# Kernel tuning notes

Measured on AMD Instinct MI355X. Metric: run time of the kernel, lower is better.

## Reference

```python
import jax, jax.numpy as jnp
import numpy as np

B, S, D, E, K = 2, 2048, 1024, 8, 2
H = 4 * D  # FFN hidden


def setup_inputs() -> dict:
    key = jax.random.key(0)
    ks = jax.random.split(key, 6)
    x = jax.random.normal(ks[0], (B, S, D), dtype=jnp.float32)
    # xavier-uniform gate
    lim_g = np.sqrt(6.0 / (D + E)).astype(np.float32)
    W_gate = jax.random.uniform(ks[1], (D, E), minval=-lim_g, maxval=lim_g, dtype=jnp.float32)
    # per-expert FFN params, stacked on leading expert axis
    lim1 = np.sqrt(1.0 / D).astype(np.float32)
    lim2 = np.sqrt(1.0 / H).astype(np.float32)
    W1 = jax.random.uniform(ks[2], (E, D, H), minval=-lim1, maxval=lim1, dtype=jnp.float32)
    b1 = jax.random.uniform(ks[3], (E, H), minval=-lim1, maxval=lim1, dtype=jnp.float32)
    W2 = jax.random.uniform(ks[4], (E, H, D), minval=-lim2, maxval=lim2, dtype=jnp.float32)
    b2 = jax.random.uniform(ks[5], (E, D), minval=-lim2, maxval=lim2, dtype=jnp.float32)
    return {"x": x, "W_gate": W_gate, "W1": W1, "b1": b1, "W2": W2, "b2": b2}


def reference(x, W_gate, W1, b1, W2, b2):
    # gating: topk mask then softmax over kept logits
    gate = jnp.einsum('bsd,de->bse', x, W_gate)                      # [B,S,E]
    kth = jax.lax.top_k(gate, K)[0][..., -1:]                        # k-th largest [B,S,1]
    mask = jax.nn.softmax(jnp.where(gate >= kth, gate, -jnp.inf), axis=-1)
    # all-experts FFN (faithful to original dense compute)
    h = jax.nn.relu(jnp.einsum('bsd,edh->bseh', x, W1) + b1)         # [B,S,E,H]
    y = jnp.einsum('bseh,ehd->bsed', h, W2) + b2                     # [B,S,E,D]
    # masked MEAN over experts (original uses .mean, i.e. divides by E)
    return (y * mask[..., None]).mean(axis=-2)                       # [B,S,D]
```

## Files before the change

### kernel.cpp

```cpp
#include <hip/hip_runtime.h>
#include <stdint.h>
#include <stddef.h>

#define TOK   4096
#define DDIM  1024
#define EXP   8
#define HDIM  4096

typedef __bf16 bf16x8 __attribute__((ext_vector_type(8)));
typedef __bf16 bf16x4 __attribute__((ext_vector_type(4)));
typedef __bf16 bf16x2 __attribute__((ext_vector_type(2)));
typedef float  f32x4  __attribute__((ext_vector_type(4)));

#define OFF_COUNTS 0ull
#define OFF_PREFIX 256ull
#define OFF_PERM   512ull
#define OFF_WGT    (OFF_PERM + 131072ull)
#define OFF_XBF    (OFF_WGT + 131072ull)
#define OFF_W1T    (OFF_XBF + 8388608ull)
#define OFF_W2T    (OFF_W1T + 67108864ull)
#define OFF_HBF    (OFF_W2T + 67108864ull)
#define OFF_T2E    (OFF_HBF + 68157440ull)

__device__ __forceinline__ void load16_lds(const void* g, void* l) {
  __builtin_amdgcn_global_load_lds((__attribute__((address_space(1))) void*)g,
                                   (__attribute__((address_space(3))) void*)l,
                                   16, 0, 0);
}

__global__ __launch_bounds__(256) void prep_kernel(
    const float* __restrict__ W1, const float* __restrict__ W2,
    __bf16* __restrict__ W1t, __bf16* __restrict__ W2t,
    const float* __restrict__ x, const float* __restrict__ Wg,
    __bf16* __restrict__ x_bf, int* __restrict__ counts,
    int* __restrict__ perm, float* __restrict__ wgt,
    int4* __restrict__ tok2exp)
{
  __shared__ __align__(16) float tile[2112];
  const int bid = blockIdx.x;
  const int tid = threadIdx.x;

  if (bid < 64) {
    const int lane = tid & 63;
    const int wid  = tid >> 6;

    int*   lcnt   = (int*)tile;
    int*   gbase  = lcnt + 8;
    int*   rec_e  = gbase + 8;
    int*   rec_p  = rec_e + 64;
    float* rec_w0 = (float*)(rec_p + 64);
    float* rec_w1 = rec_w0 + 64;

    if (tid < 8) lcnt[tid] = 0;
    __syncthreads();

#pragma unroll 1
    for (int i = 0; i < 16; ++i) {
      const int li = wid * 16 + i;
      const int t  = bid * 64 + li;
      const float* xr = x + (size_t)t * DDIM;

      float acc[EXP];
#pragma unroll
      for (int e = 0; e < EXP; ++e) acc[e] = 0.f;

#pragma unroll
      for (int it = 0; it < 4; ++it) {
        const int d0 = it * 256 + lane * 4;
        float4 xv = *(const float4*)(xr + d0);
        bf16x4 xb = { (__bf16)xv.x, (__bf16)xv.y, (__bf16)xv.z, (__bf16)xv.w };
        *(bf16x4*)(x_bf + (size_t)t * DDIM + d0) = xb;
        const float* wrow = Wg + (size_t)d0 * EXP;
        float xs[4] = { xv.x, xv.y, xv.z, xv.w };
#pragma unroll
        for (int u = 0; u < 4; ++u) {
          float4 wa = *(const float4*)(wrow + u * 8);
          float4 wb = *(const float4*)(wrow + u * 8 + 4);
          acc[0] += xs[u] * wa.x; acc[1] += xs[u] * wa.y;
          acc[2] += xs[u] * wa.z; acc[3] += xs[u] * wa.w;
          acc[4] += xs[u] * wb.x; acc[5] += xs[u] * wb.y;
          acc[6] += xs[u] * wb.z; acc[7] += xs[u] * wb.w;
        }
      }
#pragma unroll
      for (int e = 0; e < EXP; ++e) {
        float v = acc[e];
#pragma unroll
        for (int s = 32; s > 0; s >>= 1) v += __shfl_down(v, s, 64);
        acc[e] = v;
      }
      if (lane == 0) {
        int e0 = 0; float g0 = acc[0];
#pragma unroll
        for (int e = 1; e < EXP; ++e) if (acc[e] > g0) { g0 = acc[e]; e0 = e; }
        int e1 = 0; float g1 = -3.4e38f;
#pragma unroll
        for (int e = 0; e < EXP; ++e) if (e != e0 && acc[e] > g1) { g1 = acc[e]; e1 = e; }
        float ex = __expf(g1 - g0);
        float m0 = 1.f / (1.f + ex);
        float m1 = ex  / (1.f + ex);
        int lp0 = atomicAdd(&lcnt[e0], 1);
        int lp1 = atomicAdd(&lcnt[e1], 1);
        rec_e[li]  = e0 | (e1 << 8);
        rec_p[li]  = lp0 | (lp1 << 16);
        rec_w0[li] = m0 * 0.125f;
        rec_w1[li] = m1 * 0.125f;
      }
    }
    __syncthreads();
    if (tid < 8) gbase[tid] = atomicAdd(&counts[tid], lcnt[tid]);
    __syncthreads();
    if (tid < 64) {
      const int t = bid * 64 + tid;
      const int ee = rec_e[tid], pp = rec_p[tid];
      const int e0 = ee & 0xff, e1 = ee >> 8;
      const int p0 = gbase[e0] + (pp & 0xffff);
      const int p1 = gbase[e1] + (pp >> 16);
      perm[e0 * TOK + p0] = t;  wgt[e0 * TOK + p0] = rec_w0[tid];
      perm[e1 * TOK + p1] = t;  wgt[e1 * TOK + p1] = rec_w1[tid];
      tok2exp[t] = make_int4(e0, p0, e1, p1);
    }
    return;
  }

  const int tb    = bid - 64;
  const int which = tb >> 13;
  const int e     = (tb >> 10) & 7;
  const int t10   = tb & 1023;
  const float* src; __bf16* dst; int Kd, Nd, tk, tn;
  if (which == 0) { Kd = 1024; Nd = 4096; src = W1; dst = W1t; tk = t10 & 15; tn = t10 >> 4; }
  else            { Kd = 4096; Nd = 1024; src = W2; dst = W2t; tk = t10 >> 4; tn = t10 & 15; }
  const int k0 = tk * 64, n0 = tn * 64;
  src += ((size_t)e * Kd + k0) * Nd + n0;
  dst += ((size_t)e * Nd + n0) * Kd + k0;

  char* tb8 = (char*)tile;
  const int lr2 = (tid >> 4) * 2;
  const int lc  = (tid & 15) * 4;
#pragma unroll
  for (int p = 0; p < 2; ++p) {
    const int r = p * 32 + lr2;
    float4 va = *(const float4*)(src + (size_t)r * Nd + lc);
    float4 vb = *(const float4*)(src + (size_t)(r + 1) * Nd + lc);
    float a4[4] = { va.x, va.y, va.z, va.w };
    float b4[4] = { vb.x, vb.y, vb.z, vb.w };
#pragma unroll
    for (int j = 0; j < 4; ++j) {
      const int n = lc + j;
      bf16x2 w = { (__bf16)a4[j], (__bf16)b4[j] };
      *(bf16x2*)(tb8 + n * 128 + ((r * 2) ^ (((n >> 2) & 7) << 4))) = w;
    }
  }
  __syncthreads();
  const int n2 = tid >> 2, cb = tid & 3;
  const int sw = (n2 >> 2) & 7;
#pragma unroll
  for (int h = 0; h < 2; ++h) {
    const int c = cb + h * 4;
    bf16x8 o = *(const bf16x8*)(tb8 + n2 * 128 + ((c ^ sw) << 4));
    *(bf16x8*)(dst + (size_t)n2 * Kd + c * 8) = o;
  }
}

__global__ __launch_bounds__(256, 2) void gemm1_kernel(
    const __bf16* __restrict__ x_bf, const __bf16* __restrict__ W1t,
    const float* __restrict__ b1, __bf16* __restrict__ h_bf,
    const int* __restrict__ perm, const int* __restrict__ counts)
{
  const int bid = blockIdx.x;
  const int e   = bid >> 10;
  const int mt  = (bid >> 5) & 31;
  const int nt  = bid & 31;
  const int cnt = counts[e];
  if (mt * 128 >= cnt) return;
  int pfx = 0;
#pragma unroll
  for (int i = 0; i < EXP; ++i) if (i < e) pfx += counts[i];

  __shared__ __align__(16) __bf16 As[2][4096];
  __shared__ __align__(16) __bf16 Bs[2][4096];

  const int tid  = threadIdx.x;
  const int lane = tid & 63, wid = tid >> 6;
  const int wm = wid & 1, wn = wid >> 1;
  const int qd = lane >> 4, l15 = lane & 15;

  const int rA0 = tid >> 2, rA1 = rA0 + 64;
  const int pA0 = (tid & 3) ^ ((rA0 >> 1) & 3);
  const int pA1 = (tid & 3) ^ ((rA1 >> 1) & 3);
  int mA0 = mt * 128 + rA0; if (mA0 >= cnt) mA0 = cnt - 1;
  int mA1 = mt * 128 + rA1; if (mA1 >= cnt) mA1 = cnt - 1;
  const int tok0 = perm[e * TOK + mA0];
  const int tok1 = perm[e * TOK + mA1];
  const __bf16* gA0 = x_bf + (size_t)tok0 * DDIM + pA0 * 8;
  const __bf16* gA1 = x_bf + (size_t)tok1 * DDIM + pA1 * 8;
  const __bf16* Wte = W1t + (size_t)e * HDIM * DDIM;
  const __bf16* gB0 = Wte + (size_t)(nt * 128 + rA0) * DDIM + pA0 * 8;
  const __bf16* gB1 = Wte + (size_t)(nt * 128 + rA1) * DDIM + pA1 * 8;

#define STAGE1(buf, kk) do { \
    load16_lds(gA0 + (kk), &As[buf][tid * 8]); \
    load16_lds(gA1 + (kk), &As[buf][(tid + 256) * 8]); \
    load16_lds(gB0 + (kk), &Bs[buf][tid * 8]); \
    load16_lds(gB1 + (kk), &Bs[buf][(tid + 256) * 8]); \
  } while (0)

#define COMPUTE1(buf) do { \
    bf16x8 af[4], bfr[4]; \
    _Pragma("unroll") \
    for (int i = 0; i < 4; ++i) { \
      int r = wm * 64 + i * 16 + l15; \
      int ch = r * 4 + (qd ^ ((r >> 1) & 3)); \
      af[i] = *(const bf16x8*)(&As[buf][ch * 8]); \
    } \
    _Pragma("unroll") \
    for (int j = 0; j < 4; ++j) { \
      int r = wn * 64 + j * 16 + l15; \
      int ch = r * 4 + (qd ^ ((r >> 1) & 3)); \
      bfr[j] = *(const bf16x8*)(&Bs[buf][ch * 8]); \
    } \
    _Pragma("unroll") \
    for (int i = 0; i < 4; ++i) \
      _Pragma("unroll") \
      for (int j = 0; j < 4; ++j) \
        acc[i][j] = __builtin_amdgcn_mfma_f32_16x16x32_bf16(af[i], bfr[j], acc[i][j], 0, 0, 0); \
  } while (0)

  f32x4 acc[4][4] = {};

  STAGE1(0, 0);
  int cur = 0;
#pragma unroll 1
  for (int it = 0; it < 31; ++it) {
    STAGE1(cur ^ 1, (it + 1) * 32);
    asm volatile("s_waitcnt vmcnt(4)" ::: "memory");
    __builtin_amdgcn_sched_barrier(0);
    __builtin_amdgcn_s_barrier();
    __builtin_amdgcn_sched_barrier(0);
    COMPUTE1(cur);
    __builtin_amdgcn_sched_barrier(0);
    __builtin_amdgcn_s_barrier();
    __builtin_amdgcn_sched_barrier(0);
    cur ^= 1;
  }
  asm volatile("s_waitcnt vmcnt(0)" ::: "memory");
  __builtin_amdgcn_sched_barrier(0);
  __builtin_amdgcn_s_barrier();
  __builtin_amdgcn_sched_barrier(0);
  COMPUTE1(cur);
#undef STAGE1
#undef COMPUTE1

  const float* b1e = b1 + (size_t)e * HDIM;
#pragma unroll
  for (int i = 0; i < 4; ++i) {
#pragma unroll
    for (int v = 0; v < 4; ++v) {
      const int rl = wm * 64 + i * 16 + qd * 4 + v;
      const int m  = mt * 128 + rl;
      if (m < cnt) {
        __bf16* hrow = h_bf + (size_t)(pfx + m) * HDIM;
#pragma unroll
        for (int j = 0; j < 4; ++j) {
          const int col = nt * 128 + wn * 64 + j * 16 + l15;
          float hv = acc[i][j][v] + b1e[col];
          hv = fmaxf(hv, 0.f);
          hrow[col] = (__bf16)hv;
        }
      }
    }
  }
}

__global__ __launch_bounds__(256, 2) void gemm2_kernel(
    const __bf16* __restrict__ h_bf, const __bf16* __restrict__ W2t,
    __bf16* __restrict__ Y,
    const int* __restrict__ counts)
{
  const int bid = blockIdx.x;
  const int ks  = bid & 3;
  const int nt  = (bid >> 2) & 7;
  const int mt  = (bid >> 5) & 31;
  const int e   = bid >> 10;
  const int cnt = counts[e];
  if (mt * 128 >= cnt) return;
  int pfx = 0;
#pragma unroll
  for (int i = 0; i < EXP; ++i) if (i < e) pfx += counts[i];

  __shared__ __align__(16) __bf16 As[2][4096];
  __shared__ __align__(16) __bf16 Bs[2][4096];

  const int tid  = threadIdx.x;
  const int lane = tid & 63, wid = tid >> 6;
  const int wm = wid & 1, wn = wid >> 1;
  const int qd = lane >> 4, l15 = lane & 15;

  const int rA0 = tid >> 2, rA1 = rA0 + 64;
  const int pA0 = (tid & 3) ^ ((rA0 >> 1) & 3);
  const int pA1 = (tid & 3) ^ ((rA1 >> 1) & 3);
  const __bf16* gA0 = h_bf + (size_t)(pfx + mt * 128 + rA0) * HDIM + pA0 * 8;
  const __bf16* gA1 = h_bf + (size_t)(pfx + mt * 128 + rA1) * HDIM + pA1 * 8;
  const __bf16* Wte = W2t + (size_t)e * DDIM * HDIM;
  const __bf16* gB0 = Wte + (size_t)(nt * 128 + rA0) * HDIM + pA0 * 8;
  const __bf16* gB1 = Wte + (size_t)(nt * 128 + rA1) * HDIM + pA1 * 8;

#define STAGE2(buf, kk) do { \
    load16_lds(gA0 + (kk), &As[buf][tid * 8]); \
    load16_lds(gA1 + (kk), &As[buf][(tid + 256) * 8]); \
    load16_lds(gB0 + (kk), &Bs[buf][tid * 8]); \
    load16_lds(gB1 + (kk), &Bs[buf][(tid + 256) * 8]); \
  } while (0)

#define COMPUTE2(buf) do { \
    bf16x8 af[4], bfr[4]; \
    _Pragma("unroll") \
    for (int i = 0; i < 4; ++i) { \
      int r = wm * 64 + i * 16 + l15; \
      int ch = r * 4 + (qd ^ ((r >> 1) & 3)); \
      af[i] = *(const bf16x8*)(&As[buf][ch * 8]); \
    } \
    _Pragma("unroll") \
    for (int j = 0; j < 4; ++j) { \
      int r = wn * 64 + j * 16 + l15; \
      int ch = r * 4 + (qd ^ ((r >> 1) & 3)); \
      bfr[j] = *(const bf16x8*)(&Bs[buf][ch * 8]); \
    } \
    _Pragma("unroll") \
    for (int i = 0; i < 4; ++i) \
      _Pragma("unroll") \
      for (int j = 0; j < 4; ++j) \
        acc[i][j] = __builtin_amdgcn_mfma_f32_16x16x32_bf16(af[i], bfr[j], acc[i][j], 0, 0, 0); \
  } while (0)

  f32x4 acc[4][4] = {};

  const int kbeg = ks * (HDIM / 4);
  STAGE2(0, kbeg);
  int cur = 0;
#pragma unroll 1
  for (int it = 0; it < 31; ++it) {
    STAGE2(cur ^ 1, kbeg + (it + 1) * 32);
    asm volatile("s_waitcnt vmcnt(4)" ::: "memory");
    __builtin_amdgcn_sched_barrier(0);
    __builtin_amdgcn_s_barrier();
    __builtin_amdgcn_sched_barrier(0);
    COMPUTE2(cur);
    __builtin_amdgcn_sched_barrier(0);
    __builtin_amdgcn_s_barrier();
    __builtin_amdgcn_sched_barrier(0);
    cur ^= 1;
  }
  asm volatile("s_waitcnt vmcnt(0)" ::: "memory");
  __builtin_amdgcn_sched_barrier(0);
  __builtin_amdgcn_s_barrier();
  __builtin_amdgcn_sched_barrier(0);
  COMPUTE2(cur);
#undef STAGE2
#undef COMPUTE2

  __bf16* Ys = Y + (size_t)ks * (2 * TOK) * DDIM;
#pragma unroll
  for (int i = 0; i < 4; ++i) {
#pragma unroll
    for (int v = 0; v < 4; ++v) {
      const int rl = wm * 64 + i * 16 + qd * 4 + v;
      const int m  = mt * 128 + rl;
      if (m < cnt) {
        __bf16* yrow = Ys + (size_t)(pfx + m) * DDIM;
#pragma unroll
        for (int j = 0; j < 4; ++j) {
          const int col = nt * 128 + wn * 64 + j * 16 + l15;
          yrow[col] = (__bf16)acc[i][j][v];
        }
      }
    }
  }
}

__global__ __launch_bounds__(256) void combine_kernel(
    const __bf16* __restrict__ Y, const float* __restrict__ b2,
    const float* __restrict__ wgt, const int4* __restrict__ tok2exp,
    const int* __restrict__ counts, float* __restrict__ out)
{
  const int t = blockIdx.x;
  const int c = threadIdx.x * 4;
  const int4 m = tok2exp[t];
  int base0 = 0, base1 = 0;
#pragma unroll
  for (int i = 0; i < EXP; ++i) {
    int cc = counts[i];
    if (i < m.x) base0 += cc;
    if (i < m.z) base1 += cc;
  }
  const int g0 = base0 + m.y;
  const int g1 = base1 + m.w;
  const float w0 = wgt[m.x * TOK + m.y];
  const float w1 = wgt[m.z * TOK + m.w];
  const size_t slab = (size_t)(2 * TOK) * DDIM;

  float s0x = 0.f, s0y = 0.f, s0z = 0.f, s0w = 0.f;
  float s1x = 0.f, s1y = 0.f, s1z = 0.f, s1w = 0.f;
#pragma unroll
  for (int s = 0; s < 4; ++s) {
    bf16x4 a = *(const bf16x4*)(Y + s * slab + (size_t)g0 * DDIM + c);
    bf16x4 b = *(const bf16x4*)(Y + s * slab + (size_t)g1 * DDIM + c);
    s0x += (float)a[0]; s0y += (float)a[1]; s0z += (float)a[2]; s0w += (float)a[3];
    s1x += (float)b[0]; s1y += (float)b[1]; s1z += (float)b[2]; s1w += (float)b[3];
  }
  float4 be0 = *(const float4*)(b2 + (size_t)m.x * DDIM + c);
  float4 be1 = *(const float4*)(b2 + (size_t)m.z * DDIM + c);
  float4 r;
  r.x = w0 * (s0x + be0.x) + w1 * (s1x + be1.x);
  r.y = w0 * (s0y + be0.y) + w1 * (s1y + be1.y);
  r.z = w0 * (s0z + be0.z) + w1 * (s1z + be1.z);
  r.w = w0 * (s0w + be0.w) + w1 * (s1w + be1.w);
  *(float4*)(out + (size_t)t * DDIM + c) = r;
}

extern "C" void kernel_launch(void* const* d_in, const int* in_sizes, int n_in,
                              void* d_out, int out_size, void* d_ws, size_t ws_size,
                              hipStream_t stream)
{
  const float* x  = (const float*)d_in[0];
  const float* Wg = (const float*)d_in[1];
  const float* W1 = (const float*)d_in[2];
  const float* b1 = (const float*)d_in[3];
  const float* W2 = (const float*)d_in[4];
  const float* b2 = (const float*)d_in[5];
  float* out = (float*)d_out;

  char* ws = (char*)d_ws;
  int*    counts  = (int*)(ws + OFF_COUNTS);
  int*    perm    = (int*)(ws + OFF_PERM);
  float*  wgt     = (float*)(ws + OFF_WGT);
  __bf16* x_bf    = (__bf16*)(ws + OFF_XBF);
  __bf16* W1t     = (__bf16*)(ws + OFF_W1T);
  __bf16* W2t     = (__bf16*)(ws + OFF_W2T);
  __bf16* h_bf    = (__bf16*)(ws + OFF_HBF);
  int4*   tok2exp = (int4*)(ws + OFF_T2E);
  __bf16* Y       = (__bf16*)(ws + OFF_W1T);

  hipMemsetAsync(counts, 0, 256, stream);

  prep_kernel<<<64 + 16384, 256, 0, stream>>>(W1, W2, W1t, W2t,
                                              x, Wg, x_bf, counts, perm, wgt, tok2exp);
  gemm1_kernel<<<EXP * 32 * 32, 256, 0, stream>>>(x_bf, W1t, b1, h_bf, perm, counts);
  gemm2_kernel<<<EXP * 32 * 8 * 4, 256, 0, stream>>>(h_bf, W2t, Y, counts);
  combine_kernel<<<TOK, 256, 0, stream>>>(Y, b2, wgt, tok2exp, counts, out);
}
```

Baseline: 520.9 us.

## Load B fragments directly into registers and coarsen weight transpose blocks

Both GEMM kernels stop staging the weight (B) tile through LDS. Each lane now loads its MFMA B fragment straight from global memory into registers, with a one-step register prefetch, and the waitcnt is adjusted to match. This halves LDS usage and drops the B LDS reads, but each wave now issues uncoalesced 16-byte loads per row and there is no longer any cross-wave sharing of B through LDS. Separately, the weight transpose in the prep kernel is coarsened so each block handles 8 tiles, cutting the block count from 16384 to 2048.

After: 668.7 us. 28.4% more time.

```diff
diff --git a/kernel.cpp b/kernel.cpp
--- a/kernel.cpp
+++ b/kernel.cpp
@@ -26,6 +26,37 @@
   __builtin_amdgcn_global_load_lds((__attribute__((address_space(1))) void*)g,
                                    (__attribute__((address_space(3))) void*)l,
                                    16, 0, 0);
+}
+
+__device__ __forceinline__ void transpose_tile64(const float* __restrict__ src,
+                                                 __bf16* __restrict__ dst,
+                                                 int Nd, int Kd, char* tb8, int tid)
+{
+  const int lr2 = (tid >> 4) * 2;
+  const int lc  = (tid & 15) * 4;
+#pragma unroll
+  for (int p = 0; p < 2; ++p) {
+    const int r = p * 32 + lr2;
+    float4 va = *(const float4*)(src + (size_t)r * Nd + lc);
+    float4 vb = *(const float4*)(src + (size_t)(r + 1) * Nd + lc);
+    float a4[4] = { va.x, va.y, va.z, va.w };
+    float b4[4] = { vb.x, vb.y, vb.z, vb.w };
+#pragma unroll
+    for (int j = 0; j < 4; ++j) {
+      const int n = lc + j;
+      bf16x2 w = { (__bf16)a4[j], (__bf16)b4[j] };
+      *(bf16x2*)(tb8 + n * 128 + ((r * 2) ^ (((n >> 2) & 7) << 4))) = w;
+    }
+  }
+  __syncthreads();
+  const int n2 = tid >> 2, cb = tid & 3;
+  const int sw = (n2 >> 2) & 7;
+#pragma unroll
+  for (int h = 0; h < 2; ++h) {
+    const int c = cb + h * 4;
+    bf16x8 o = *(const bf16x8*)(tb8 + n2 * 128 + ((c ^ sw) << 4));
+    *(bf16x8*)(dst + (size_t)n2 * Kd + c * 8) = o;
+  }
 }
 
 __global__ __launch_bounds__(256) void prep_kernel(
@@ -123,42 +154,32 @@
     return;
   }
 
-  const int tb    = bid - 64;
-  const int which = tb >> 13;
-  const int e     = (tb >> 10) & 7;
-  const int t10   = tb & 1023;
-  const float* src; __bf16* dst; int Kd, Nd, tk, tn;
-  if (which == 0) { Kd = 1024; Nd = 4096; src = W1; dst = W1t; tk = t10 & 15; tn = t10 >> 4; }
-  else            { Kd = 4096; Nd = 1024; src = W2; dst = W2t; tk = t10 >> 4; tn = t10 & 15; }
-  const int k0 = tk * 64, n0 = tn * 64;
-  src += ((size_t)e * Kd + k0) * Nd + n0;
-  dst += ((size_t)e * Nd + n0) * Kd + k0;
-
-  char* tb8 = (char*)tile;
-  const int lr2 = (tid >> 4) * 2;
-  const int lc  = (tid & 15) * 4;
-#pragma unroll
-  for (int p = 0; p < 2; ++p) {
-    const int r = p * 32 + lr2;
-    float4 va = *(const float4*)(src + (size_t)r * Nd + lc);
-    float4 vb = *(const float4*)(src + (size_t)(r + 1) * Nd + lc);
-    float a4[4] = { va.x, va.y, va.z, va.w };
-    float b4[4] = { vb.x, vb.y, vb.z, vb.w };
-#pragma unroll
-    for (int j = 0; j < 4; ++j) {
-      const int n = lc + j;
-      bf16x2 w = { (__bf16)a4[j], (__bf16)b4[j] };
-      *(bf16x2*)(tb8 + n * 128 + ((r * 2) ^ (((n >> 2) & 7) << 4))) = w;
-    }
-  }
-  __syncthreads();
-  const int n2 = tid >> 2, cb = tid & 3;
-  const int sw = (n2 >> 2) & 7;
-#pragma unroll
-  for (int h = 0; h < 2; ++h) {
-    const int c = cb + h * 4;
-    bf16x8 o = *(const bf16x8*)(tb8 + n2 * 128 + ((c ^ sw) << 4));
-    *(bf16x8*)(dst + (size_t)n2 * Kd + c * 8) = o;
+  const int tb = bid - 64;
+  if (tb < 1024) {
+    const int e  = tb >> 7;
+    const int r7 = tb & 127;
+    const int tn = r7 >> 1, kg = r7 & 1;
+#pragma unroll 1
+    for (int i = 0; i < 8; ++i) {
+      const int tk = kg * 8 + i;
+      const float* src = W1 + ((size_t)e * 1024 + tk * 64) * 4096 + tn * 64;
+      __bf16*      dst = W1t + ((size_t)e * 4096 + tn * 64) * 1024 + tk * 64;
+      transpose_tile64(src, dst, 4096, 1024, (char*)tile, tid);
+      __syncthreads();
+    }
+  } else {
+    const int idx = tb - 1024;
+    const int e  = idx >> 7;
+    const int r7 = idx & 127;
+    const int tn = r7 >> 3, kg = r7 & 7;
+#pragma unroll 1
+    for (int i = 0; i < 8; ++i) {
+      const int tk = kg * 8 + i;
+      const float* src = W2 + ((size_t)e * 4096 + tk * 64) * 1024 + tn * 64;
+      __bf16*      dst = W2t + ((size_t)e * 1024 + tn * 64) * 4096 + tk * 64;
+      transpose_tile64(src, dst, 1024, 4096, (char*)tile, tid);
+      __syncthreads();
+    }
   }
 }
 
@@ -178,7 +199,6 @@
   for (int i = 0; i < EXP; ++i) if (i < e) pfx += counts[i];
 
   __shared__ __align__(16) __bf16 As[2][4096];
-  __shared__ __align__(16) __bf16 Bs[2][4096];
 
   const int tid  = threadIdx.x;
   const int lane = tid & 63, wid = tid >> 6;
@@ -195,18 +215,18 @@
   const __bf16* gA0 = x_bf + (size_t)tok0 * DDIM + pA0 * 8;
   const __bf16* gA1 = x_bf + (size_t)tok1 * DDIM + pA1 * 8;
   const __bf16* Wte = W1t + (size_t)e * HDIM * DDIM;
-  const __bf16* gB0 = Wte + (size_t)(nt * 128 + rA0) * DDIM + pA0 * 8;
-  const __bf16* gB1 = Wte + (size_t)(nt * 128 + rA1) * DDIM + pA1 * 8;
-
-#define STAGE1(buf, kk) do { \
+  const __bf16* gB[4];
+#pragma unroll
+  for (int j = 0; j < 4; ++j)
+    gB[j] = Wte + (size_t)(nt * 128 + wn * 64 + j * 16 + l15) * DDIM + qd * 8;
+
+#define STAGEA1(buf, kk) do { \
     load16_lds(gA0 + (kk), &As[buf][tid * 8]); \
     load16_lds(gA1 + (kk), &As[buf][(tid + 256) * 8]); \
-    load16_lds(gB0 + (kk), &Bs[buf][tid * 8]); \
-    load16_lds(gB1 + (kk), &Bs[buf][(tid + 256) * 8]); \
   } while (0)
 
 #define COMPUTE1(buf) do { \
-    bf16x8 af[4], bfr[4]; \
+    bf16x8 af[4]; \
     _Pragma("unroll") \
     for (int i = 0; i < 4; ++i) { \
       int r = wm * 64 + i * 16 + l15; \
@@ -214,30 +234,32 @@
       af[i] = *(const bf16x8*)(&As[buf][ch * 8]); \
     } \
     _Pragma("unroll") \
-    for (int j = 0; j < 4; ++j) { \
-      int r = wn * 64 + j * 16 + l15; \
-      int ch = r * 4 + (qd ^ ((r >> 1) & 3)); \
-      bfr[j] = *(const bf16x8*)(&Bs[buf][ch * 8]); \
-    } \
-    _Pragma("unroll") \
     for (int i = 0; i < 4; ++i) \
       _Pragma("unroll") \
       for (int j = 0; j < 4; ++j) \
-        acc[i][j] = __builtin_amdgcn_mfma_f32_16x16x32_bf16(af[i], bfr[j], acc[i][j], 0, 0, 0); \
+        acc[i][j] = __builtin_amdgcn_mfma_f32_16x16x32_bf16(af[i], bcur[j], acc[i][j], 0, 0, 0); \
   } while (0)
 
   f32x4 acc[4][4] = {};
-
-  STAGE1(0, 0);
+  bf16x8 bcur[4], bnxt[4];
+
+  STAGEA1(0, 0);
+#pragma unroll
+  for (int j = 0; j < 4; ++j) bcur[j] = *(const bf16x8*)(gB[j]);
+
   int cur = 0;
 #pragma unroll 1
   for (int it = 0; it < 31; ++it) {
-    STAGE1(cur ^ 1, (it + 1) * 32);
-    asm volatile("s_waitcnt vmcnt(4)" ::: "memory");
+    STAGEA1(cur ^ 1, (it + 1) * 32);
+#pragma unroll
+    for (int j = 0; j < 4; ++j) bnxt[j] = *(const bf16x8*)(gB[j] + (it + 1) * 32);
+    asm volatile("s_waitcnt vmcnt(6)" ::: "memory");
     __builtin_amdgcn_sched_barrier(0);
     __builtin_amdgcn_s_barrier();
     __builtin_amdgcn_sched_barrier(0);
     COMPUTE1(cur);
+#pragma unroll
+    for (int j = 0; j < 4; ++j) bcur[j] = bnxt[j];
     __builtin_amdgcn_sched_barrier(0);
     __builtin_amdgcn_s_barrier();
     __builtin_amdgcn_sched_barrier(0);
@@ -248,7 +270,7 @@
   __builtin_amdgcn_s_barrier();
   __builtin_amdgcn_sched_barrier(0);
   COMPUTE1(cur);
-#undef STAGE1
+#undef STAGEA1
 #undef COMPUTE1
 
   const float* b1e = b1 + (size_t)e * HDIM;
@@ -289,7 +311,6 @@
   for (int i = 0; i < EXP; ++i) if (i < e) pfx += counts[i];
 
   __shared__ __align__(16) __bf16 As[2][4096];
-  __shared__ __align__(16) __bf16 Bs[2][4096];
 
   const int tid  = threadIdx.x;
   const int lane = tid & 63, wid = tid >> 6;
@@ -302,18 +323,18 @@
   const __bf16* gA0 = h_bf + (size_t)(pfx + mt * 128 + rA0) * HDIM + pA0 * 8;
   const __bf16* gA1 = h_bf + (size_t)(pfx + mt * 128 + rA1) * HDIM + pA1 * 8;
   const __bf16* Wte = W2t + (size_t)e * DDIM * HDIM;
-  const __bf16* gB0 = Wte + (size_t)(nt * 128 + rA0) * HDIM + pA0 * 8;
-  const __bf16* gB1 = Wte + (size_t)(nt * 128 + rA1) * HDIM + pA1 * 8;
-
-#define STAGE2(buf, kk) do { \
+  const __bf16* gB[4];
+#pragma unroll
+  for (int j = 0; j < 4; ++j)
+    gB[j] = Wte + (size_t)(nt * 128 + wn * 64 + j * 16 + l15) * HDIM + qd * 8;
+
+#define STAGEA2(buf, kk) do { \
     load16_lds(gA0 + (kk), &As[buf][tid * 8]); \
     load16_lds(gA1 + (kk), &As[buf][(tid + 256) * 8]); \
-    load16_lds(gB0 + (kk), &Bs[buf][tid * 8]); \
-    load16_lds(gB1 + (kk), &Bs[buf][(tid + 256) * 8]); \
   } while (0)
 
 #define COMPUTE2(buf) do { \
-    bf16x8 af[4], bfr[4]; \
+    bf16x8 af[4]; \
     _Pragma("unroll") \
     for (int i = 0; i < 4; ++i) { \
       int r = wm * 64 + i * 16 + l15; \
@@ -321,31 +342,33 @@
       af[i] = *(const bf16x8*)(&As[buf][ch * 8]); \
     } \
     _Pragma("unroll") \
-    for (int j = 0; j < 4; ++j) { \
-      int r = wn * 64 + j * 16 + l15; \
-      int ch = r * 4 + (qd ^ ((r >> 1) & 3)); \
-      bfr[j] = *(const bf16x8*)(&Bs[buf][ch * 8]); \
-    } \
-    _Pragma("unroll") \
     for (int i = 0; i < 4; ++i) \
       _Pragma("unroll") \
       for (int j = 0; j < 4; ++j) \
-        acc[i][j] = __builtin_amdgcn_mfma_f32_16x16x32_bf16(af[i], bfr[j], acc[i][j], 0, 0, 0); \
+        acc[i][j] = __builtin_amdgcn_mfma_f32_16x16x32_bf16(af[i], bcur[j], acc[i][j], 0, 0, 0); \
   } while (0)
 
   f32x4 acc[4][4] = {};
+  bf16x8 bcur[4], bnxt[4];
 
   const int kbeg = ks * (HDIM / 4);
-  STAGE2(0, kbeg);
+  STAGEA2(0, kbeg);
+#pragma unroll
+  for (int j = 0; j < 4; ++j) bcur[j] = *(const bf16x8*)(gB[j] + kbeg);
+
   int cur = 0;
 #pragma unroll 1
   for (int it = 0; it < 31; ++it) {
-    STAGE2(cur ^ 1, kbeg + (it + 1) * 32);
-    asm volatile("s_waitcnt vmcnt(4)" ::: "memory");
+    STAGEA2(cur ^ 1, kbeg + (it + 1) * 32);
+#pragma unroll
+    for (int j = 0; j < 4; ++j) bnxt[j] = *(const bf16x8*)(gB[j] + kbeg + (it + 1) * 32);
+    asm volatile("s_waitcnt vmcnt(6)" ::: "memory");
     __builtin_amdgcn_sched_barrier(0);
     __builtin_amdgcn_s_barrier();
     __builtin_amdgcn_sched_barrier(0);
     COMPUTE2(cur);
+#pragma unroll
+    for (int j = 0; j < 4; ++j) bcur[j] = bnxt[j];
     __builtin_amdgcn_sched_barrier(0);
     __builtin_amdgcn_s_barrier();
     __builtin_amdgcn_sched_barrier(0);
@@ -356,7 +379,7 @@
   __builtin_amdgcn_s_barrier();
   __builtin_amdgcn_sched_barrier(0);
   COMPUTE2(cur);
-#undef STAGE2
+#undef STAGEA2
 #undef COMPUTE2
 
   __bf16* Ys = Y + (size_t)ks * (2 * TOK) * DDIM;
@@ -443,8 +466,8 @@
 
   hipMemsetAsync(counts, 0, 256, stream);
 
-  prep_kernel<<<64 + 16384, 256, 0, stream>>>(W1, W2, W1t, W2t,
-                                              x, Wg, x_bf, counts, perm, wgt, tok2exp);
+  prep_kernel<<<64 + 2048, 256, 0, stream>>>(W1, W2, W1t, W2t,
+                                             x, Wg, x_bf, counts, perm, wgt, tok2exp);
   gemm1_kernel<<<EXP * 32 * 32, 256, 0, stream>>>(x_bf, W1t, b1, h_bf, perm, counts);
   gemm2_kernel<<<EXP * 32 * 8 * 4, 256, 0, stream>>>(h_bf, W2t, Y, counts);
   combine_kernel<<<TOK, 256, 0, stream>>>(Y, b2, wgt, tok2exp, counts, out);
```

## Pre-pack expert weights in MFMA fragment order and load B directly to registers

Applied to the files above, without the earlier changes.

The prep kernel now writes W1/W2 as bf16 in a per-wave MFMA fragment layout, so each lane's 16-byte B operand is contiguous. The GEMM kernels drop the B shared-memory tiles and load B fragments from global memory straight into registers, double-buffered across k-steps alongside the LDS-staged A tiles. This removes the B staging traffic through LDS and the LDS reads for B, at the cost of more register pressure. It also means redundant global reads of B across the two wm waves, since each wave fetches its own copy.

Result: slower. 541.8 us (+4.0%).

```diff
diff --git a/kernel.cpp b/kernel.cpp
--- a/kernel.cpp
+++ b/kernel.cpp
@@ -22,15 +22,50 @@
 #define OFF_HBF    (OFF_W2T + 67108864ull)
 #define OFF_T2E    (OFF_HBF + 68157440ull)
 
+#define FRAG_E_STRIDE (4194304ull)
+
 __device__ __forceinline__ void load16_lds(const void* g, void* l) {
   __builtin_amdgcn_global_load_lds((__attribute__((address_space(1))) void*)g,
                                    (__attribute__((address_space(3))) void*)l,
                                    16, 0, 0);
 }
 
+__device__ __forceinline__ void transpose_frag64(const float* __restrict__ src,
+                                                 __bf16* __restrict__ dstFe, int Nd, int KC,
+                                                 int k0, int n0, char* tb8, int tid)
+{
+  const int lr2 = (tid >> 4) * 2;
+  const int lc  = (tid & 15) * 4;
+#pragma unroll
+  for (int p = 0; p < 2; ++p) {
+    const int r = p * 32 + lr2;
+    float4 va = *(const float4*)(src + (size_t)r * Nd + lc);
+    float4 vb = *(const float4*)(src + (size_t)(r + 1) * Nd + lc);
+    float a4[4] = { va.x, va.y, va.z, va.w };
+    float b4[4] = { vb.x, vb.y, vb.z, vb.w };
+#pragma unroll
+    for (int j = 0; j < 4; ++j) {
+      const int n = lc + j;
+      bf16x2 w = { (__bf16)a4[j], (__bf16)b4[j] };
+      *(bf16x2*)(tb8 + n * 128 + ((r * 2) ^ (((n >> 2) & 7) << 4))) = w;
+    }
+  }
+  __syncthreads();
+  const int w = tid >> 6, l = tid & 63;
+  const int n2 = w * 16 + (l & 15);
+  const int sw = (n2 >> 2) & 7;
+  const size_t fragrow = (size_t)((n0 >> 4) + w) * KC + (k0 >> 5);
+#pragma unroll
+  for (int h = 0; h < 2; ++h) {
+    const int c = h * 4 + (l >> 4);
+    bf16x8 o = *(const bf16x8*)(tb8 + n2 * 128 + ((c ^ sw) << 4));
+    *(bf16x8*)(dstFe + (fragrow + h) * 512 + l * 8) = o;
+  }
+}
+
 __global__ __launch_bounds__(256) void prep_kernel(
     const float* __restrict__ W1, const float* __restrict__ W2,
-    __bf16* __restrict__ W1t, __bf16* __restrict__ W2t,
+    __bf16* __restrict__ W1f, __bf16* __restrict__ W2f,
     const float* __restrict__ x, const float* __restrict__ Wg,
     __bf16* __restrict__ x_bf, int* __restrict__ counts,
     int* __restrict__ perm, float* __restrict__ wgt,
@@ -127,43 +162,21 @@
   const int which = tb >> 13;
   const int e     = (tb >> 10) & 7;
   const int t10   = tb & 1023;
-  const float* src; __bf16* dst; int Kd, Nd, tk, tn;
-  if (which == 0) { Kd = 1024; Nd = 4096; src = W1; dst = W1t; tk = t10 & 15; tn = t10 >> 4; }
-  else            { Kd = 4096; Nd = 1024; src = W2; dst = W2t; tk = t10 >> 4; tn = t10 & 15; }
-  const int k0 = tk * 64, n0 = tn * 64;
-  src += ((size_t)e * Kd + k0) * Nd + n0;
-  dst += ((size_t)e * Nd + n0) * Kd + k0;
-
-  char* tb8 = (char*)tile;
-  const int lr2 = (tid >> 4) * 2;
-  const int lc  = (tid & 15) * 4;
-#pragma unroll
-  for (int p = 0; p < 2; ++p) {
-    const int r = p * 32 + lr2;
-    float4 va = *(const float4*)(src + (size_t)r * Nd + lc);
-    float4 vb = *(const float4*)(src + (size_t)(r + 1) * Nd + lc);
-    float a4[4] = { va.x, va.y, va.z, va.w };
-    float b4[4] = { vb.x, vb.y, vb.z, vb.w };
-#pragma unroll
-    for (int j = 0; j < 4; ++j) {
-      const int n = lc + j;
-      bf16x2 w = { (__bf16)a4[j], (__bf16)b4[j] };
-      *(bf16x2*)(tb8 + n * 128 + ((r * 2) ^ (((n >> 2) & 7) << 4))) = w;
-    }
-  }
-  __syncthreads();
-  const int n2 = tid >> 2, cb = tid & 3;
-  const int sw = (n2 >> 2) & 7;
-#pragma unroll
-  for (int h = 0; h < 2; ++h) {
-    const int c = cb + h * 4;
-    bf16x8 o = *(const bf16x8*)(tb8 + n2 * 128 + ((c ^ sw) << 4));
-    *(bf16x8*)(dst + (size_t)n2 * Kd + c * 8) = o;
+  if (which == 0) {
+    const int tk = t10 & 15, tn = t10 >> 4;
+    const float* src = W1 + ((size_t)e * 1024 + tk * 64) * 4096 + tn * 64;
+    transpose_frag64(src, W1f + (size_t)e * FRAG_E_STRIDE, 4096, 32,
+                     tk * 64, tn * 64, (char*)tile, tid);
+  } else {
+    const int tk = t10 >> 4, tn = t10 & 15;
+    const float* src = W2 + ((size_t)e * 4096 + tk * 64) * 1024 + tn * 64;
+    transpose_frag64(src, W2f + (size_t)e * FRAG_E_STRIDE, 1024, 128,
+                     tk * 64, tn * 64, (char*)tile, tid);
   }
 }
 
 __global__ __launch_bounds__(256, 2) void gemm1_kernel(
-    const __bf16* __restrict__ x_bf, const __bf16* __restrict__ W1t,
+    const __bf16* __restrict__ x_bf, const __bf16* __restrict__ W1f,
     const float* __restrict__ b1, __bf16* __restrict__ h_bf,
     const int* __restrict__ perm, const int* __restrict__ counts)
 {
@@ -178,7 +191,6 @@
   for (int i = 0; i < EXP; ++i) if (i < e) pfx += counts[i];
 
   __shared__ __align__(16) __bf16 As[2][4096];
-  __shared__ __align__(16) __bf16 Bs[2][4096];
 
   const int tid  = threadIdx.x;
   const int lane = tid & 63, wid = tid >> 6;
@@ -194,19 +206,24 @@
   const int tok1 = perm[e * TOK + mA1];
   const __bf16* gA0 = x_bf + (size_t)tok0 * DDIM + pA0 * 8;
   const __bf16* gA1 = x_bf + (size_t)tok1 * DDIM + pA1 * 8;
-  const __bf16* Wte = W1t + (size_t)e * HDIM * DDIM;
-  const __bf16* gB0 = Wte + (size_t)(nt * 128 + rA0) * DDIM + pA0 * 8;
-  const __bf16* gB1 = Wte + (size_t)(nt * 128 + rA1) * DDIM + pA1 * 8;
-
-#define STAGE1(buf, kk) do { \
+  const __bf16* Bf = W1f + (size_t)e * FRAG_E_STRIDE + lane * 8;
+  size_t fb[4];
+#pragma unroll
+  for (int j = 0; j < 4; ++j)
+    fb[j] = (size_t)((nt * 8 + wn * 4 + j) * 32) * 512;
+
+#define STAGEA(buf, kk) do { \
     load16_lds(gA0 + (kk), &As[buf][tid * 8]); \
     load16_lds(gA1 + (kk), &As[buf][(tid + 256) * 8]); \
-    load16_lds(gB0 + (kk), &Bs[buf][tid * 8]); \
-    load16_lds(gB1 + (kk), &Bs[buf][(tid + 256) * 8]); \
-  } while (0)
-
-#define COMPUTE1(buf) do { \
-    bf16x8 af[4], bfr[4]; \
+  } while (0)
+
+#define LOADB(dst, s) do { \
+    _Pragma("unroll") \
+    for (int j = 0; j < 4; ++j) dst[j] = *(const bf16x8*)(Bf + fb[j] + (size_t)(s) * 512); \
+  } while (0)
+
+#define COMPUTE(buf, bb) do { \
+    bf16x8 af[4]; \
     _Pragma("unroll") \
     for (int i = 0; i < 4; ++i) { \
       int r = wm * 64 + i * 16 + l15; \
@@ -214,42 +231,42 @@
       af[i] = *(const bf16x8*)(&As[buf][ch * 8]); \
     } \
     _Pragma("unroll") \
-    for (int j = 0; j < 4; ++j) { \
-      int r = wn * 64 + j * 16 + l15; \
-      int ch = r * 4 + (qd ^ ((r >> 1) & 3)); \
-      bfr[j] = *(const bf16x8*)(&Bs[buf][ch * 8]); \
-    } \
-    _Pragma("unroll") \
     for (int i = 0; i < 4; ++i) \
       _Pragma("unroll") \
       for (int j = 0; j < 4; ++j) \
-        acc[i][j] = __builtin_amdgcn_mfma_f32_16x16x32_bf16(af[i], bfr[j], acc[i][j], 0, 0, 0); \
-  } while (0)
+        acc[i][j] = __builtin_amdgcn_mfma_f32_16x16x32_bf16(af[i], bb[j], acc[i][j], 0, 0, 0); \
+  } while (0)
+
+#define SB __builtin_amdgcn_sched_barrier(0)
 
   f32x4 acc[4][4] = {};
-
-  STAGE1(0, 0);
-  int cur = 0;
+  bf16x8 b0[4], b1r[4];
+
+  STAGEA(0, 0); LOADB(b0, 0);
 #pragma unroll 1
-  for (int it = 0; it < 31; ++it) {
-    STAGE1(cur ^ 1, (it + 1) * 32);
-    asm volatile("s_waitcnt vmcnt(4)" ::: "memory");
-    __builtin_amdgcn_sched_barrier(0);
-    __builtin_amdgcn_s_barrier();
-    __builtin_amdgcn_sched_barrier(0);
-    COMPUTE1(cur);
-    __builtin_amdgcn_sched_barrier(0);
-    __builtin_amdgcn_s_barrier();
-    __builtin_amdgcn_sched_barrier(0);
-    cur ^= 1;
-  }
-  asm volatile("s_waitcnt vmcnt(0)" ::: "memory");
-  __builtin_amdgcn_sched_barrier(0);
-  __builtin_amdgcn_s_barrier();
-  __builtin_amdgcn_sched_barrier(0);
-  COMPUTE1(cur);
-#undef STAGE1
-#undef COMPUTE1
+  for (int s = 0; s < 30; s += 2) {
+    STAGEA(1, (s + 1) * 32); LOADB(b1r, s + 1);
+    SB; asm volatile("s_waitcnt vmcnt(6)" ::: "memory"); SB;
+    __builtin_amdgcn_s_barrier(); SB;
+    COMPUTE(0, b0);
+    SB; __builtin_amdgcn_s_barrier(); SB;
+    STAGEA(0, (s + 2) * 32); LOADB(b0, s + 2);
+    SB; asm volatile("s_waitcnt vmcnt(6)" ::: "memory"); SB;
+    __builtin_amdgcn_s_barrier(); SB;
+    COMPUTE(1, b1r);
+    SB; __builtin_amdgcn_s_barrier(); SB;
+  }
+  STAGEA(1, 31 * 32); LOADB(b1r, 31);
+  SB; asm volatile("s_waitcnt vmcnt(6)" ::: "memory"); SB;
+  __builtin_amdgcn_s_barrier(); SB;
+  COMPUTE(0, b0);
+  SB; __builtin_amdgcn_s_barrier(); SB;
+  asm volatile("s_waitcnt vmcnt(0)" ::: "memory"); SB;
+  __builtin_amdgcn_s_barrier(); SB;
+  COMPUTE(1, b1r);
+#undef STAGEA
+#undef LOADB
+#undef COMPUTE
 
   const float* b1e = b1 + (size_t)e * HDIM;
 #pragma unroll
@@ -273,7 +290,7 @@
 }
 
 __global__ __launch_bounds__(256, 2) void gemm2_kernel(
-    const __bf16* __restrict__ h_bf, const __bf16* __restrict__ W2t,
+    const __bf16* __restrict__ h_bf, const __bf16* __restrict__ W2f,
     __bf16* __restrict__ Y,
     const int* __restrict__ counts)
 {
@@ -289,7 +306,6 @@
   for (int i = 0; i < EXP; ++i) if (i < e) pfx += counts[i];
 
   __shared__ __align__(16) __bf16 As[2][4096];
-  __shared__ __align__(16) __bf16 Bs[2][4096];
 
   const int tid  = threadIdx.x;
   const int lane = tid & 63, wid = tid >> 6;
@@ -301,19 +317,25 @@
   const int pA1 = (tid & 3) ^ ((rA1 >> 1) & 3);
   const __bf16* gA0 = h_bf + (size_t)(pfx + mt * 128 + rA0) * HDIM + pA0 * 8;
   const __bf16* gA1 = h_bf + (size_t)(pfx + mt * 128 + rA1) * HDIM + pA1 * 8;
-  const __bf16* Wte = W2t + (size_t)e * DDIM * HDIM;
-  const __bf16* gB0 = Wte + (size_t)(nt * 128 + rA0) * HDIM + pA0 * 8;
-  const __bf16* gB1 = Wte + (size_t)(nt * 128 + rA1) * HDIM + pA1 * 8;
-
-#define STAGE2(buf, kk) do { \
+  const __bf16* Bf = W2f + (size_t)e * FRAG_E_STRIDE + lane * 8;
+  const int kbeg = ks * (HDIM / 4);
+  size_t fb[4];
+#pragma unroll
+  for (int j = 0; j < 4; ++j)
+    fb[j] = (size_t)((nt * 8 + wn * 4 + j) * 128 + ks * 32) * 512;
+
+#define STAGEA(buf, kk) do { \
     load16_lds(gA0 + (kk), &As[buf][tid * 8]); \
     load16_lds(gA1 + (kk), &As[buf][(tid + 256) * 8]); \
-    load16_lds(gB0 + (kk), &Bs[buf][tid * 8]); \
-    load16_lds(gB1 + (kk), &Bs[buf][(tid + 256) * 8]); \
-  } while (0)
-
-#define COMPUTE2(buf) do { \
-    bf16x8 af[4], bfr[4]; \
+  } while (0)
+
+#define LOADB(dst, s) do { \
+    _Pragma("unroll") \
+    for (int j = 0; j < 4; ++j) dst[j] = *(const bf16x8*)(Bf + fb[j] + (size_t)(s) * 512); \
+  } while (0)
+
+#define COMPUTE(buf, bb) do { \
+    bf16x8 af[4]; \
     _Pragma("unroll") \
     for (int i = 0; i < 4; ++i) { \
       int r = wm * 64 + i * 16 + l15; \
@@ -321,43 +343,41 @@
       af[i] = *(const bf16x8*)(&As[buf][ch * 8]); \
     } \
     _Pragma("unroll") \
-    for (int j = 0; j < 4; ++j) { \
-      int r = wn * 64 + j * 16 + l15; \
-      int ch = r * 4 + (qd ^ ((r >> 1) & 3)); \
-      bfr[j] = *(const bf16x8*)(&Bs[buf][ch * 8]); \
-    } \
-    _Pragma("unroll") \
     for (int i = 0; i < 4; ++i) \
       _Pragma("unroll") \
       for (int j = 0; j < 4; ++j) \
-        acc[i][j] = __builtin_amdgcn_mfma_f32_16x16x32_bf16(af[i], bfr[j], acc[i][j], 0, 0, 0); \
+        acc[i][j] = __builtin_amdgcn_mfma_f32_16x16x32_bf16(af[i], bb[j], acc[i][j], 0, 0, 0); \
   } while (0)
 
   f32x4 acc[4][4] = {};
-
-  const int kbeg = ks * (HDIM / 4);
-  STAGE2(0, kbeg);
-  int cur = 0;
+  bf16x8 b0[4], b1r[4];
+
+  STAGEA(0, kbeg); LOADB(b0, 0);
 #pragma unroll 1
-  for (int it = 0; it < 31; ++it) {
-    STAGE2(cur ^ 1, kbeg + (it + 1) * 32);
-    asm volatile("s_waitcnt vmcnt(4)" ::: "memory");
-    __builtin_amdgcn_sched_barrier(0);
-    __builtin_amdgcn_s_barrier();
-    __builtin_amdgcn_sched_barrier(0);
-    COMPUTE2(cur);
-    __builtin_amdgcn_sched_barrier(0);
-    __builtin_amdgcn_s_barrier();
-    __builtin_amdgcn_sched_barrier(0);
-    cur ^= 1;
-  }
-  asm volatile("s_waitcnt vmcnt(0)" ::: "memory");
-  __builtin_amdgcn_sched_barrier(0);
-  __builtin_amdgcn_s_barrier();
-  __builtin_amdgcn_sched_barrier(0);
-  COMPUTE2(cur);
-#undef STAGE2
-#undef COMPUTE2
+  for (int s = 0; s < 30; s += 2) {
+    STAGEA(1, kbeg + (s + 1) * 32); LOADB(b1r, s + 1);
+    SB; asm volatile("s_waitcnt vmcnt(6)" ::: "memory"); SB;
+    __builtin_amdgcn_s_barrier(); SB;
+    COMPUTE(0, b0);
+    SB; __builtin_amdgcn_s_barrier(); SB;
+    STAGEA(0, kbeg + (s + 2) * 32); LOADB(b0, s + 2);
+    SB; asm volatile("s_waitcnt vmcnt(6)" ::: "memory"); SB;
+    __builtin_amdgcn_s_barrier(); SB;
+    COMPUTE(1, b1r);
+    SB; __builtin_amdgcn_s_barrier(); SB;
+  }
+  STAGEA(1, kbeg + 31 * 32); LOADB(b1r, 31);
+  SB; asm volatile("s_waitcnt vmcnt(6)" ::: "memory"); SB;
+  __builtin_amdgcn_s_barrier(); SB;
+  COMPUTE(0, b0);
+  SB; __builtin_amdgcn_s_barrier(); SB;
+  asm volatile("s_waitcnt vmcnt(0)" ::: "memory"); SB;
+  __builtin_amdgcn_s_barrier(); SB;
+  COMPUTE(1, b1r);
+#undef STAGEA
+#undef LOADB
+#undef COMPUTE
+#undef SB
 
   __bf16* Ys = Y + (size_t)ks * (2 * TOK) * DDIM;
 #pragma unroll
@@ -435,17 +455,17 @@
   int*    perm    = (int*)(ws + OFF_PERM);
   float*  wgt     = (float*)(ws + OFF_WGT);
   __bf16* x_bf    = (__bf16*)(ws + OFF_XBF);
-  __bf16* W1t     = (__bf16*)(ws + OFF_W1T);
-  __bf16* W2t     = (__bf16*)(ws + OFF_W2T);
+  __bf16* W1f     = (__bf16*)(ws + OFF_W1T);
+  __bf16* W2f     = (__bf16*)(ws + OFF_W2T);
   __bf16* h_bf    = (__bf16*)(ws + OFF_HBF);
   int4*   tok2exp = (int4*)(ws + OFF_T2E);
   __bf16* Y       = (__bf16*)(ws + OFF_W1T);
 
   hipMemsetAsync(counts, 0, 256, stream);
 
-  prep_kernel<<<64 + 16384, 256, 0, stream>>>(W1, W2, W1t, W2t,
+  prep_kernel<<<64 + 16384, 256, 0, stream>>>(W1, W2, W1f, W2f,
                                               x, Wg, x_bf, counts, perm, wgt, tok2exp);
-  gemm1_kernel<<<EXP * 32 * 32, 256, 0, stream>>>(x_bf, W1t, b1, h_bf, perm, counts);
-  gemm2_kernel<<<EXP * 32 * 8 * 4, 256, 0, stream>>>(h_bf, W2t, Y, counts);
+  gemm1_kernel<<<EXP * 32 * 32, 256, 0, stream>>>(x_bf, W1f, b1, h_bf, perm, counts);
+  gemm2_kernel<<<EXP * 32 * 8 * 4, 256, 0, stream>>>(h_bf, W2f, Y, counts);
   combine_kernel<<<TOK, 256, 0, stream>>>(Y, b2, wgt, tok2exp, counts, out);
 }
```
